# Performance work log

Measured on AMD Instinct MI355X. Metric: run time of the kernel, lower is better.

Reference implementation:

```python
import jax, jax.numpy as jnp
import numpy as np

N_NODES = 100000
N_EDGES = 1600000


def gcn_conv(x, W, b, src, dst, n):
    # PyG GCNConv: x @ W, add self-loops, symmetric deg^{-1/2} normalization,
    # sum-aggregate messages from src into dst, then add bias.
    h = x @ W  # [N, out]
    loops = jnp.arange(n, dtype=src.dtype)
    s = jnp.concatenate([src, loops])
    d = jnp.concatenate([dst, loops])
    deg = jax.ops.segment_sum(jnp.ones_like(d, dtype=h.dtype), d, num_segments=n)
    dinv = 1.0 / jnp.sqrt(deg)  # deg >= 1 thanks to self-loops
    norm = dinv[s] * dinv[d]  # [E + N]
    msg = h[s] * norm[:, None]
    out = jax.ops.segment_sum(msg, d, num_segments=n)
    return out + b


def setup_inputs() -> dict:
    key = jax.random.key(0)
    k1, k2, k3, k4 = jax.random.split(key, 4)
    x = jax.random.normal(k1, (N_NODES, 64), dtype=jnp.float32)
    edge_index = jax.random.randint(k2, (2, N_EDGES), 0, N_NODES, dtype=jnp.int64)
    W1 = jax.random.normal(k3, (64, 32), dtype=jnp.float32) * (1.0 / np.sqrt(64))
    b1 = jnp.zeros((32,), dtype=jnp.float32)
    W2 = jax.random.normal(k4, (32, 16), dtype=jnp.float32) * (1.0 / np.sqrt(32))
    b2 = jnp.zeros((16,), dtype=jnp.float32)
    return {"x": x, "edge_index": edge_index, "W1": W1, "b1": b1, "W2": W2, "b2": b2}


def reference(x, edge_index, W1, b1, W2, b2):
    n = x.shape[0]
    src, dst = edge_index[0], edge_index[1]
    h = gcn_conv(x, W1, b1, src, dst, n)
    h = jax.nn.relu(h)
    h = gcn_conv(h, W2, b2, src, dst, n)
    return jax.nn.log_softmax(h, axis=1)
```

## Files before the change

### kernel.cpp

```cpp
#include <hip/hip_runtime.h>
#include <hip/hip_bf16.h>


#define FEAT_IN 64
#define FEAT_H  32
#define FEAT_O  16
#define MAXNB   512
#define PART_G  256
#define MAXSNB  128

__device__ __forceinline__ float2 upk_bf2(unsigned w) {
    return make_float2(__uint_as_float(w << 16), __uint_as_float(w & 0xFFFF0000u));
}

__global__ void k_hist(const int* __restrict__ dst, int e,
                       int* __restrict__ hist, int G, int NBk) {
    __shared__ int lh[MAXNB];
    int t = threadIdx.x, g = blockIdx.x;
    for (int i = t; i < NBk; i += 256) lh[i] = 0;
    __syncthreads();
    int chunk = (e + G - 1) / G;
    int beg = g * chunk, end = min(e, beg + chunk);
    for (int i = beg + t; i < end; i += 256) atomicAdd(&lh[dst[i] >> 8], 1);
    __syncthreads();
    for (int i = t; i < NBk; i += 256) hist[(size_t)i * G + g] = lh[i];
}

__global__ void k_scan1(const int* __restrict__ in, int* __restrict__ out,
                        int* __restrict__ bsum, int len) {
    __shared__ int s[256];
    int t = threadIdx.x;
    int base = blockIdx.x * 1024 + t * 4;
    int a0 = (base + 0) < len ? in[base + 0] : 0;
    int a1 = (base + 1) < len ? in[base + 1] : 0;
    int a2 = (base + 2) < len ? in[base + 2] : 0;
    int a3 = (base + 3) < len ? in[base + 3] : 0;
    int tsum = a0 + a1 + a2 + a3;
    s[t] = tsum;
    __syncthreads();
    for (int off = 1; off < 256; off <<= 1) {
        int x = (t >= off) ? s[t - off] : 0;
        __syncthreads();
        s[t] += x;
        __syncthreads();
    }
    int ex = s[t] - tsum;
    if (base + 0 < len) out[base + 0] = ex;
    if (base + 1 < len) out[base + 1] = ex + a0;
    if (base + 2 < len) out[base + 2] = ex + a0 + a1;
    if (base + 3 < len) out[base + 3] = ex + a0 + a1 + a2;
    if (t == 255) bsum[blockIdx.x] = s[255];
}

__device__ __forceinline__ void scan_bsum(const int* __restrict__ bsum, int snb,
                                          int* __restrict__ sps, int t) {
    if (t < snb) sps[t] = bsum[t];
    __syncthreads();
    if (t == 0) {
        int acc = 0;
        for (int i = 0; i < snb; ++i) { int v = sps[i]; sps[i] = acc; acc += v; }
    }
    __syncthreads();
}

__global__ void k_partition(const int* __restrict__ src, const int* __restrict__ dst, int e,
                            const int* __restrict__ base, const int* __restrict__ bsum,
                            int snb, int* __restrict__ part, int G, int NBk) {
    __shared__ int cur[MAXNB];
    __shared__ int sps[MAXSNB];
    int t = threadIdx.x, g = blockIdx.x;
    scan_bsum(bsum, snb, sps, t);
    for (int i = t; i < NBk; i += 256) {
        size_t idx = (size_t)i * G + g;
        cur[i] = base[idx] + sps[idx >> 10];
    }
    __syncthreads();
    int chunk = (e + G - 1) / G;
    int beg = g * chunk, end = min(e, beg + chunk);
    for (int i = beg + t; i < end; i += 256) {
        int s_ = src[i], d_ = dst[i];
        int pos = atomicAdd(&cur[d_ >> 8], 1);
        part[pos] = s_ | ((d_ & 255) << 24);
    }
}

__global__ void k_bucket_csr(const int* __restrict__ part, const int* __restrict__ base,
                             const int* __restrict__ bsum, int snb, int e, int G, int NBk,
                             int n, int* __restrict__ row_start, int* __restrict__ col,
                             float* __restrict__ dinv) {
    __shared__ int cnt[256], spre[256], cur[256], ssc[256];
    __shared__ int sps[MAXSNB];
    int t = threadIdx.x, b = blockIdx.x;
    scan_bsum(bsum, snb, sps, t);
    size_t ib = (size_t)b * G;
    size_t ie = (size_t)(b + 1) * G;
    int beg = base[ib] + sps[ib >> 10];
    int end = (b == NBk - 1) ? e : (base[ie] + sps[ie >> 10]);
    cnt[t] = 0; cur[t] = 0;
    __syncthreads();
    for (int j = beg + t; j < end; j += 256) atomicAdd(&cnt[((unsigned)part[j]) >> 24], 1);
    __syncthreads();
    int v = cnt[t];
    ssc[t] = v;
    __syncthreads();
    for (int off = 1; off < 256; off <<= 1) {
        int x = (t >= off) ? ssc[t - off] : 0;
        __syncthreads();
        ssc[t] += x;
        __syncthreads();
    }
    spre[t] = ssc[t] - v;
    int node = b * 256 + t;
    if (node < n) {
        row_start[node] = beg + spre[t];
        dinv[node] = rsqrtf((float)v + 1.0f);
    }
    if (b == NBk - 1 && t == 0) row_start[n] = e;
    __syncthreads();
    for (int j = beg + t; j < end; j += 256) {
        int r = part[j];
        int dl = ((unsigned)r) >> 24;
        int off = atomicAdd(&cur[dl], 1);
        col[beg + spre[dl] + off] = r & 0x00FFFFFF;
    }
}

__global__ void k_gemm1(const float* __restrict__ x, const float* __restrict__ W1,
                        const float* __restrict__ dinv,
                        __hip_bfloat162* __restrict__ h1s2, int n) {
    __shared__ float sW[FEAT_IN * FEAT_H];
    __shared__ float sx[16][FEAT_IN + 1];
    int t = threadIdx.x;
    for (int i = t; i < FEAT_IN * FEAT_H; i += 256) sW[i] = W1[i];
#pragma unroll
    for (int tile = 0; tile < 2; ++tile) {
        int nodeBase = blockIdx.x * 32 + tile * 16;
        __syncthreads();
        {
            int xn = t >> 4, c = t & 15;
            int node = nodeBase + xn;
            if (node < n) {
                float4 v = ((const float4*)x)[(size_t)node * 16 + c];
                sx[xn][c * 4 + 0] = v.x; sx[xn][c * 4 + 1] = v.y;
                sx[xn][c * 4 + 2] = v.z; sx[xn][c * 4 + 3] = v.w;
            }
        }
        __syncthreads();
        int nl = t >> 4, g = t & 15;
        int node = nodeBase + nl;
        if (node < n) {
            float a0 = 0.0f, a1 = 0.0f;
#pragma unroll
            for (int k = 0; k < FEAT_IN; ++k) {
                float s = sx[nl][k];
                a0 += s * sW[k * FEAT_H + 2 * g];
                a1 += s * sW[k * FEAT_H + 2 * g + 1];
            }
            float dv = dinv[node];
            __hip_bfloat162 o;
            o.x = __float2bfloat16(a0 * dv);
            o.y = __float2bfloat16(a1 * dv);
            h1s2[(size_t)node * 16 + g] = o;
        }
    }
}

__global__ void k_gather1_gemm2(const int* __restrict__ row_start, const int* __restrict__ col,
                                const uint4* __restrict__ h1q, const float* __restrict__ W2,
                                const float* __restrict__ b1,
                                const float* __restrict__ dinv,
                                __hip_bfloat162* __restrict__ h2s2, int n) {
    __shared__ float sW[FEAT_H * FEAT_O];
    __shared__ float sb1[FEAT_H];
    __shared__ float sz[64][FEAT_H + 1];
    int t = threadIdx.x;
    for (int i = t; i < FEAT_H * FEAT_O; i += 256) sW[i] = W2[i];
    if (t < FEAT_H) sb1[t] = b1[t];
    __syncthreads();

    int g = t >> 2, l = t & 3;
    int d = blockIdx.x * 64 + g;
    if (d < n) {
        float a[8];
        {
            uint4 u = h1q[(size_t)d * 4 + l];
            float2 p;
            p = upk_bf2(u.x); a[0] = p.x; a[1] = p.y;
            p = upk_bf2(u.y); a[2] = p.x; a[3] = p.y;
            p = upk_bf2(u.z); a[4] = p.x; a[5] = p.y;
            p = upk_bf2(u.w); a[6] = p.x; a[7] = p.y;
        }
        int beg = row_start[d], end = row_start[d + 1];
        int j = beg;
        for (; j + 4 <= end; j += 4) {
            int c0 = col[j + 0], c1 = col[j + 1], c2 = col[j + 2], c3 = col[j + 3];
            uint4 u0 = h1q[(size_t)c0 * 4 + l];
            uint4 u1 = h1q[(size_t)c1 * 4 + l];
            uint4 u2 = h1q[(size_t)c2 * 4 + l];
            uint4 u3 = h1q[(size_t)c3 * 4 + l];
            float2 p;
            p = upk_bf2(u0.x); a[0] += p.x; a[1] += p.y;
            p = upk_bf2(u0.y); a[2] += p.x; a[3] += p.y;
            p = upk_bf2(u0.z); a[4] += p.x; a[5] += p.y;
            p = upk_bf2(u0.w); a[6] += p.x; a[7] += p.y;
            p = upk_bf2(u1.x); a[0] += p.x; a[1] += p.y;
            p = upk_bf2(u1.y); a[2] += p.x; a[3] += p.y;
            p = upk_bf2(u1.z); a[4] += p.x; a[5] += p.y;
            p = upk_bf2(u1.w); a[6] += p.x; a[7] += p.y;
            p = upk_bf2(u2.x); a[0] += p.x; a[1] += p.y;
            p = upk_bf2(u2.y); a[2] += p.x; a[3] += p.y;
            p = upk_bf2(u2.z); a[4] += p.x; a[5] += p.y;
            p = upk_bf2(u2.w); a[6] += p.x; a[7] += p.y;
            p = upk_bf2(u3.x); a[0] += p.x; a[1] += p.y;
            p = upk_bf2(u3.y); a[2] += p.x; a[3] += p.y;
            p = upk_bf2(u3.z); a[4] += p.x; a[5] += p.y;
            p = upk_bf2(u3.w); a[6] += p.x; a[7] += p.y;
        }
        for (; j < end; ++j) {
            uint4 u = h1q[(size_t)col[j] * 4 + l];
            float2 p;
            p = upk_bf2(u.x); a[0] += p.x; a[1] += p.y;
            p = upk_bf2(u.y); a[2] += p.x; a[3] += p.y;
            p = upk_bf2(u.z); a[4] += p.x; a[5] += p.y;
            p = upk_bf2(u.w); a[6] += p.x; a[7] += p.y;
        }
        float dv = dinv[d];
#pragma unroll
        for (int k = 0; k < 8; ++k)
            sz[g][l * 8 + k] = fmaxf(dv * a[k] + sb1[l * 8 + k], 0.0f);
    }
    __syncthreads();
#pragma unroll
    for (int it = 0; it < 2; ++it) {
        int nl = (t >> 3) + it * 32;
        int m = t & 7;
        int node = blockIdx.x * 64 + nl;
        if (node < n) {
            float a0 = 0.0f, a1 = 0.0f;
#pragma unroll
            for (int f = 0; f < FEAT_H; ++f) {
                float z = sz[nl][f];
                a0 += z * sW[f * FEAT_O + 2 * m];
                a1 += z * sW[f * FEAT_O + 2 * m + 1];
            }
            float dv = dinv[node];
            __hip_bfloat162 o;
            o.x = __float2bfloat16(a0 * dv);
            o.y = __float2bfloat16(a1 * dv);
            h2s2[(size_t)node * 8 + m] = o;
        }
    }
}

__global__ void k_gather2_lsm(const int* __restrict__ row_start, const int* __restrict__ col,
                              const uint4* __restrict__ h2q, const float* __restrict__ b2,
                              const float* __restrict__ dinv,
                              float4* __restrict__ out4, int n) {
    __shared__ float sb2[FEAT_O];
    int t = threadIdx.x;
    if (t < FEAT_O) sb2[t] = b2[t];
    __syncthreads();
    int g = t >> 1, h = t & 1;
    int d = blockIdx.x * 128 + g;
    if (d >= n) return;
    float a[8];
    {
        uint4 u = h2q[(size_t)d * 2 + h];
        float2 p;
        p = upk_bf2(u.x); a[0] = p.x; a[1] = p.y;
        p = upk_bf2(u.y); a[2] = p.x; a[3] = p.y;
        p = upk_bf2(u.z); a[4] = p.x; a[5] = p.y;
        p = upk_bf2(u.w); a[6] = p.x; a[7] = p.y;
    }
    int beg = row_start[d], end = row_start[d + 1];
    int j = beg;
    for (; j + 4 <= end; j += 4) {
        int c0 = col[j + 0], c1 = col[j + 1], c2 = col[j + 2], c3 = col[j + 3];
        uint4 u0 = h2q[(size_t)c0 * 2 + h];
        uint4 u1 = h2q[(size_t)c1 * 2 + h];
        uint4 u2 = h2q[(size_t)c2 * 2 + h];
        uint4 u3 = h2q[(size_t)c3 * 2 + h];
        float2 p;
        p = upk_bf2(u0.x); a[0] += p.x; a[1] += p.y;
        p = upk_bf2(u0.y); a[2] += p.x; a[3] += p.y;
        p = upk_bf2(u0.z); a[4] += p.x; a[5] += p.y;
        p = upk_bf2(u0.w); a[6] += p.x; a[7] += p.y;
        p = upk_bf2(u1.x); a[0] += p.x; a[1] += p.y;
        p = upk_bf2(u1.y); a[2] += p.x; a[3] += p.y;
        p = upk_bf2(u1.z); a[4] += p.x; a[5] += p.y;
        p = upk_bf2(u1.w); a[6] += p.x; a[7] += p.y;
        p = upk_bf2(u2.x); a[0] += p.x; a[1] += p.y;
        p = upk_bf2(u2.y); a[2] += p.x; a[3] += p.y;
        p = upk_bf2(u2.z); a[4] += p.x; a[5] += p.y;
        p = upk_bf2(u2.w); a[6] += p.x; a[7] += p.y;
        p = upk_bf2(u3.x); a[0] += p.x; a[1] += p.y;
        p = upk_bf2(u3.y); a[2] += p.x; a[3] += p.y;
        p = upk_bf2(u3.z); a[4] += p.x; a[5] += p.y;
        p = upk_bf2(u3.w); a[6] += p.x; a[7] += p.y;
    }
    for (; j < end; ++j) {
        uint4 u = h2q[(size_t)col[j] * 2 + h];
        float2 p;
        p = upk_bf2(u.x); a[0] += p.x; a[1] += p.y;
        p = upk_bf2(u.y); a[2] += p.x; a[3] += p.y;
        p = upk_bf2(u.z); a[4] += p.x; a[5] += p.y;
        p = upk_bf2(u.w); a[6] += p.x; a[7] += p.y;
    }
    float dv = dinv[d];
    float v[8];
    float mx = -1e30f;
#pragma unroll
    for (int k = 0; k < 8; ++k) {
        v[k] = dv * a[k] + sb2[h * 8 + k];
        mx = fmaxf(mx, v[k]);
    }
    mx = fmaxf(mx, __shfl_xor(mx, 1));
    float ssum = 0.0f;
#pragma unroll
    for (int k = 0; k < 8; ++k) ssum += __expf(v[k] - mx);
    ssum += __shfl_xor(ssum, 1);
    float lg = mx + logf(ssum);
    float4 o0 = { v[0] - lg, v[1] - lg, v[2] - lg, v[3] - lg };
    float4 o1 = { v[4] - lg, v[5] - lg, v[6] - lg, v[7] - lg };
    out4[(size_t)d * 4 + h * 2 + 0] = o0;
    out4[(size_t)d * 4 + h * 2 + 1] = o1;
}

extern "C" void kernel_launch(void* const* d_in, const int* in_sizes, int n_in,
                              void* d_out, int out_size, void* d_ws, size_t ws_size,
                              hipStream_t stream) {
    const float* x  = (const float*)d_in[0];
    const int*   ei = (const int*)d_in[1];
    const float* W1 = (const float*)d_in[2];
    const float* b1 = (const float*)d_in[3];
    const float* W2 = (const float*)d_in[4];
    const float* b2 = (const float*)d_in[5];

    const int n = in_sizes[0] / FEAT_IN;
    const int e = in_sizes[1] / 2;
    const int* src = ei;
    const int* dst = ei + e;
    const int NBk = (n + 255) >> 8;
    const int G = PART_G;
    const int hlen = NBk * G;
    const int snb = (hlen + 1023) / 1024;

    int* part = (int*)d_ws;
    __hip_bfloat162* h1s2 = (__hip_bfloat162*)d_ws;
    int* col  = (int*)d_ws + e;
    __hip_bfloat162* h2s2 = (__hip_bfloat162*)(col + e);
    float* dinv = (float*)(h2s2 + 8 * (size_t)n);
    int* hist      = (int*)(dinv + n);
    int* base      = hist + hlen;
    int* bsum      = base + hlen;
    int* row_start = bsum + MAXSNB;

    k_hist<<<G, 256, 0, stream>>>(dst, e, hist, G, NBk);
    k_scan1<<<snb, 256, 0, stream>>>(hist, base, bsum, hlen);
    k_partition<<<G, 256, 0, stream>>>(src, dst, e, base, bsum, snb, part, G, NBk);
    k_bucket_csr<<<NBk, 256, 0, stream>>>(part, base, bsum, snb, e, G, NBk, n,
                                          row_start, col, dinv);

    k_gemm1<<<(n + 31) / 32, 256, 0, stream>>>(x, W1, dinv, h1s2, n);
    k_gather1_gemm2<<<(n + 63) / 64, 256, 0, stream>>>(row_start, col, (const uint4*)h1s2,
                                                       W2, b1, dinv, h2s2, n);
    k_gather2_lsm<<<(n + 127) / 128, 256, 0, stream>>>(row_start, col, (const uint4*)h2s2,
                                                       b2, dinv, (float4*)d_out, n);
}
```

Before: 184.2 us.

## Replace histogram-scan partition with fixed-capacity buckets and fuse CSR build with GEMM1

The exact prefix-scan partition (hist, scan, partition kernels) is replaced by fixed-capacity buckets of CAP slots each, with offsets claimed by global atomics in a single partition kernel. The CSR-build kernel is fused with the first GEMM, and dinv is recomputed from a per-node (start, count) pair instead of being stored. This cuts the launch count and the global round-trips, but assumes no 256-node bucket receives more than CAP edges. That holds for uniform random graphs but would overflow on skewed degree distributions. The fused kernel also processes 256 nodes of GEMM1 per block on fewer blocks, which may lower parallelism for that stage.

```diff
diff --git a/kernel.cpp b/kernel.cpp
--- a/kernel.cpp
+++ b/kernel.cpp
@@ -7,15 +7,16 @@
 #define FEAT_O  16
 #define MAXNB   512
 #define PART_G  256
-#define MAXSNB  128
+#define CAP     5120
 
 __device__ __forceinline__ float2 upk_bf2(unsigned w) {
     return make_float2(__uint_as_float(w << 16), __uint_as_float(w & 0xFFFF0000u));
 }
 
-__global__ void k_hist(const int* __restrict__ dst, int e,
-                       int* __restrict__ hist, int G, int NBk) {
+__global__ void k_part1(const int* __restrict__ src, const int* __restrict__ dst, int e,
+                        int* __restrict__ gcur, int* __restrict__ part, int G, int NBk) {
     __shared__ int lh[MAXNB];
+    __shared__ int rb[MAXNB];
     int t = threadIdx.x, g = blockIdx.x;
     for (int i = t; i < NBk; i += 256) lh[i] = 0;
     __syncthreads();
@@ -23,80 +24,34 @@
     int beg = g * chunk, end = min(e, beg + chunk);
     for (int i = beg + t; i < end; i += 256) atomicAdd(&lh[dst[i] >> 8], 1);
     __syncthreads();
-    for (int i = t; i < NBk; i += 256) hist[(size_t)i * G + g] = lh[i];
-}
-
-__global__ void k_scan1(const int* __restrict__ in, int* __restrict__ out,
-                        int* __restrict__ bsum, int len) {
-    __shared__ int s[256];
-    int t = threadIdx.x;
-    int base = blockIdx.x * 1024 + t * 4;
-    int a0 = (base + 0) < len ? in[base + 0] : 0;
-    int a1 = (base + 1) < len ? in[base + 1] : 0;
-    int a2 = (base + 2) < len ? in[base + 2] : 0;
-    int a3 = (base + 3) < len ? in[base + 3] : 0;
-    int tsum = a0 + a1 + a2 + a3;
-    s[t] = tsum;
-    __syncthreads();
-    for (int off = 1; off < 256; off <<= 1) {
-        int x = (t >= off) ? s[t - off] : 0;
-        __syncthreads();
-        s[t] += x;
-        __syncthreads();
-    }
-    int ex = s[t] - tsum;
-    if (base + 0 < len) out[base + 0] = ex;
-    if (base + 1 < len) out[base + 1] = ex + a0;
-    if (base + 2 < len) out[base + 2] = ex + a0 + a1;
-    if (base + 3 < len) out[base + 3] = ex + a0 + a1 + a2;
-    if (t == 255) bsum[blockIdx.x] = s[255];
-}
-
-__device__ __forceinline__ void scan_bsum(const int* __restrict__ bsum, int snb,
-                                          int* __restrict__ sps, int t) {
-    if (t < snb) sps[t] = bsum[t];
-    __syncthreads();
-    if (t == 0) {
-        int acc = 0;
-        for (int i = 0; i < snb; ++i) { int v = sps[i]; sps[i] = acc; acc += v; }
-    }
-    __syncthreads();
-}
-
-__global__ void k_partition(const int* __restrict__ src, const int* __restrict__ dst, int e,
-                            const int* __restrict__ base, const int* __restrict__ bsum,
-                            int snb, int* __restrict__ part, int G, int NBk) {
-    __shared__ int cur[MAXNB];
-    __shared__ int sps[MAXSNB];
-    int t = threadIdx.x, g = blockIdx.x;
-    scan_bsum(bsum, snb, sps, t);
     for (int i = t; i < NBk; i += 256) {
-        size_t idx = (size_t)i * G + g;
-        cur[i] = base[idx] + sps[idx >> 10];
-    }
-    __syncthreads();
-    int chunk = (e + G - 1) / G;
-    int beg = g * chunk, end = min(e, beg + chunk);
+        int c = lh[i];
+        rb[i] = c ? atomicAdd(&gcur[i], c) : 0;
+    }
+    __syncthreads();
+    for (int i = t; i < NBk; i += 256) lh[i] = i * CAP + rb[i];
+    __syncthreads();
     for (int i = beg + t; i < end; i += 256) {
         int s_ = src[i], d_ = dst[i];
-        int pos = atomicAdd(&cur[d_ >> 8], 1);
+        int pos = atomicAdd(&lh[d_ >> 8], 1);
         part[pos] = s_ | ((d_ & 255) << 24);
     }
 }
 
-__global__ void k_bucket_csr(const int* __restrict__ part, const int* __restrict__ base,
-                             const int* __restrict__ bsum, int snb, int e, int G, int NBk,
-                             int n, int* __restrict__ row_start, int* __restrict__ col,
-                             float* __restrict__ dinv) {
+__global__ void k_csr_gemm1(const int* __restrict__ part, const int* __restrict__ gcur,
+                            int NBk, int n,
+                            const float* __restrict__ x, const float* __restrict__ W1,
+                            int2* __restrict__ row_info, int* __restrict__ col,
+                            __hip_bfloat162* __restrict__ h1s2) {
     __shared__ int cnt[256], spre[256], cur[256], ssc[256];
-    __shared__ int sps[MAXSNB];
+    __shared__ float sdv[256];
+    __shared__ float sW[FEAT_IN * FEAT_H];
+    __shared__ float sx[16][FEAT_IN + 1];
     int t = threadIdx.x, b = blockIdx.x;
-    scan_bsum(bsum, snb, sps, t);
-    size_t ib = (size_t)b * G;
-    size_t ie = (size_t)(b + 1) * G;
-    int beg = base[ib] + sps[ib >> 10];
-    int end = (b == NBk - 1) ? e : (base[ie] + sps[ie >> 10]);
-    cnt[t] = 0; cur[t] = 0;
+    int beg = b * CAP;
+    int end = beg + gcur[b];
+    cnt[t] = 0;
+    for (int i = t; i < FEAT_IN * FEAT_H; i += 256) sW[i] = W1[i];
     __syncthreads();
     for (int j = beg + t; j < end; j += 256) atomicAdd(&cnt[((unsigned)part[j]) >> 24], 1);
     __syncthreads();
@@ -104,75 +59,64 @@
     ssc[t] = v;
     __syncthreads();
     for (int off = 1; off < 256; off <<= 1) {
-        int x = (t >= off) ? ssc[t - off] : 0;
+        int xv = (t >= off) ? ssc[t - off] : 0;
         __syncthreads();
-        ssc[t] += x;
+        ssc[t] += xv;
         __syncthreads();
     }
     spre[t] = ssc[t] - v;
+    sdv[t] = rsqrtf((float)v + 1.0f);
     int node = b * 256 + t;
-    if (node < n) {
-        row_start[node] = beg + spre[t];
-        dinv[node] = rsqrtf((float)v + 1.0f);
-    }
-    if (b == NBk - 1 && t == 0) row_start[n] = e;
+    if (node < n) row_info[node] = make_int2(beg + spre[t], v);
+    cur[t] = beg + spre[t];
     __syncthreads();
     for (int j = beg + t; j < end; j += 256) {
         int r = part[j];
         int dl = ((unsigned)r) >> 24;
         int off = atomicAdd(&cur[dl], 1);
-        col[beg + spre[dl] + off] = r & 0x00FFFFFF;
-    }
-}
-
-__global__ void k_gemm1(const float* __restrict__ x, const float* __restrict__ W1,
-                        const float* __restrict__ dinv,
-                        __hip_bfloat162* __restrict__ h1s2, int n) {
-    __shared__ float sW[FEAT_IN * FEAT_H];
-    __shared__ float sx[16][FEAT_IN + 1];
-    int t = threadIdx.x;
-    for (int i = t; i < FEAT_IN * FEAT_H; i += 256) sW[i] = W1[i];
-#pragma unroll
-    for (int tile = 0; tile < 2; ++tile) {
-        int nodeBase = blockIdx.x * 32 + tile * 16;
+        col[off] = r & 0x00FFFFFF;
+    }
+#pragma unroll 1
+    for (int tile = 0; tile < 16; ++tile) {
+        int nodeBase = b * 256 + tile * 16;
         __syncthreads();
         {
             int xn = t >> 4, c = t & 15;
-            int node = nodeBase + xn;
-            if (node < n) {
-                float4 v = ((const float4*)x)[(size_t)node * 16 + c];
-                sx[xn][c * 4 + 0] = v.x; sx[xn][c * 4 + 1] = v.y;
-                sx[xn][c * 4 + 2] = v.z; sx[xn][c * 4 + 3] = v.w;
+            int nd = nodeBase + xn;
+            if (nd < n) {
+                float4 vv = ((const float4*)x)[(size_t)nd * 16 + c];
+                sx[xn][c * 4 + 0] = vv.x; sx[xn][c * 4 + 1] = vv.y;
+                sx[xn][c * 4 + 2] = vv.z; sx[xn][c * 4 + 3] = vv.w;
             }
         }
         __syncthreads();
-        int nl = t >> 4, g = t & 15;
-        int node = nodeBase + nl;
-        if (node < n) {
+        int nl = t >> 4, gg = t & 15;
+        int nd = nodeBase + nl;
+        if (nd < n) {
             float a0 = 0.0f, a1 = 0.0f;
 #pragma unroll
             for (int k = 0; k < FEAT_IN; ++k) {
                 float s = sx[nl][k];
-                a0 += s * sW[k * FEAT_H + 2 * g];
-                a1 += s * sW[k * FEAT_H + 2 * g + 1];
+                a0 += s * sW[k * FEAT_H + 2 * gg];
+                a1 += s * sW[k * FEAT_H + 2 * gg + 1];
             }
-            float dv = dinv[node];
+            float dvn = sdv[tile * 16 + nl];
             __hip_bfloat162 o;
-            o.x = __float2bfloat16(a0 * dv);
-            o.y = __float2bfloat16(a1 * dv);
-            h1s2[(size_t)node * 16 + g] = o;
-        }
-    }
-}
-
-__global__ void k_gather1_gemm2(const int* __restrict__ row_start, const int* __restrict__ col,
+            o.x = __float2bfloat16(a0 * dvn);
+            o.y = __float2bfloat16(a1 * dvn);
+            h1s2[(size_t)nd * 16 + gg] = o;
+        }
+    }
+}
+
+__global__ void k_gather1_gemm2(const int2* __restrict__ row_info, const int* __restrict__ col,
                                 const uint4* __restrict__ h1q, const float* __restrict__ W2,
                                 const float* __restrict__ b1,
-                                const float* __restrict__ dinv,
                                 __hip_bfloat162* __restrict__ h2s2, int n) {
     __shared__ float sW[FEAT_H * FEAT_O];
     __shared__ float sb1[FEAT_H];
     __shared__ float sz[64][FEAT_H + 1];
+    __shared__ float sdv[64];
     int t = threadIdx.x;
     for (int i = t; i < FEAT_H * FEAT_O; i += 256) sW[i] = W2[i];
     if (t < FEAT_H) sb1[t] = b1[t];
@@ -190,7 +134,8 @@
             p = upk_bf2(u.z); a[4] = p.x; a[5] = p.y;
             p = upk_bf2(u.w); a[6] = p.x; a[7] = p.y;
         }
-        int beg = row_start[d], end = row_start[d + 1];
+        int2 ri = row_info[d];
+        int beg = ri.x, end = ri.x + ri.y;
         int j = beg;
         for (; j + 4 <= end; j += 4) {
             int c0 = col[j + 0], c1 = col[j + 1], c2 = col[j + 2], c3 = col[j + 3];
@@ -224,7 +169,8 @@
             p = upk_bf2(u.z); a[4] += p.x; a[5] += p.y;
             p = upk_bf2(u.w); a[6] += p.x; a[7] += p.y;
         }
-        float dv = dinv[d];
+        float dv = rsqrtf((float)ri.y + 1.0f);
+        if (l == 0) sdv[g] = dv;
 #pragma unroll
         for (int k = 0; k < 8; ++k)
             sz[g][l * 8 + k] = fmaxf(dv * a[k] + sb1[l * 8 + k], 0.0f);
@@ -243,7 +189,7 @@
                 a0 += z * sW[f * FEAT_O + 2 * m];
                 a1 += z * sW[f * FEAT_O + 2 * m + 1];
             }
-            float dv = dinv[node];
+            float dv = sdv[nl];
             __hip_bfloat162 o;
             o.x = __float2bfloat16(a0 * dv);
             o.y = __float2bfloat16(a1 * dv);
@@ -252,9 +198,8 @@
     }
 }
 
-__global__ void k_gather2_lsm(const int* __restrict__ row_start, const int* __restrict__ col,
+__global__ void k_gather2_lsm(const int2* __restrict__ row_info, const int* __restrict__ col,
                               const uint4* __restrict__ h2q, const float* __restrict__ b2,
-                              const float* __restrict__ dinv,
                               float4* __restrict__ out4, int n) {
     __shared__ float sb2[FEAT_O];
     int t = threadIdx.x;
@@ -272,7 +217,8 @@
         p = upk_bf2(u.z); a[4] = p.x; a[5] = p.y;
         p = upk_bf2(u.w); a[6] = p.x; a[7] = p.y;
     }
-    int beg = row_start[d], end = row_start[d + 1];
+    int2 ri = row_info[d];
+    int beg = ri.x, end = ri.x + ri.y;
     int j = beg;
     for (; j + 4 <= end; j += 4) {
         int c0 = col[j + 0], c1 = col[j + 1], c2 = col[j + 2], c3 = col[j + 3];
@@ -306,7 +252,7 @@
         p = upk_bf2(u.z); a[4] += p.x; a[5] += p.y;
         p = upk_bf2(u.w); a[6] += p.x; a[7] += p.y;
     }
-    float dv = dinv[d];
+    float dv = rsqrtf((float)ri.y + 1.0f);
     float v[8];
     float mx = -1e30f;
 #pragma unroll
@@ -342,28 +288,19 @@
     const int* dst = ei + e;
     const int NBk = (n + 255) >> 8;
     const int G = PART_G;
-    const int hlen = NBk * G;
-    const int snb = (hlen + 1023) / 1024;
-
-    int* part = (int*)d_ws;
-    __hip_bfloat162* h1s2 = (__hip_bfloat162*)d_ws;
-    int* col  = (int*)d_ws + e;
-    __hip_bfloat162* h2s2 = (__hip_bfloat162*)(col + e);
-    float* dinv = (float*)(h2s2 + 8 * (size_t)n);
-    int* hist      = (int*)(dinv + n);
-    int* base      = hist + hlen;
-    int* bsum      = base + hlen;
-    int* row_start = bsum + MAXSNB;
-
-    k_hist<<<G, 256, 0, stream>>>(dst, e, hist, G, NBk);
-    k_scan1<<<snb, 256, 0, stream>>>(hist, base, bsum, hlen);
-    k_partition<<<G, 256, 0, stream>>>(src, dst, e, base, bsum, snb, part, G, NBk);
-    k_bucket_csr<<<NBk, 256, 0, stream>>>(part, base, bsum, snb, e, G, NBk, n,
-                                          row_start, col, dinv);
-
-    k_gemm1<<<(n + 31) / 32, 256, 0, stream>>>(x, W1, dinv, h1s2, n);
-    k_gather1_gemm2<<<(n + 63) / 64, 256, 0, stream>>>(row_start, col, (const uint4*)h1s2,
-                                                       W2, b1, dinv, h2s2, n);
-    k_gather2_lsm<<<(n + 127) / 128, 256, 0, stream>>>(row_start, col, (const uint4*)h2s2,
-                                                       b2, dinv, (float4*)d_out, n);
-}
+
+    int*  gcur = (int*)d_ws;
+    int*  part = gcur + MAXNB;
+    int*  col  = part + (size_t)NBk * CAP;
+    int2* row_info = (int2*)(col + (size_t)NBk * CAP);
+    __hip_bfloat162* h1s2 = (__hip_bfloat162*)(row_info + n);
+    __hip_bfloat162* h2s2 = h1s2 + 16 * (size_t)n;
+
+    hipMemsetAsync(gcur, 0, (size_t)NBk * sizeof(int), stream);
+    k_part1<<<G, 256, 0, stream>>>(src, dst, e, gcur, part, G, NBk);
+    k_csr_gemm1<<<NBk, 256, 0, stream>>>(part, gcur, NBk, n, x, W1, row_info, col, h1s2);
+    k_gather1_gemm2<<<(n + 63) / 64, 256, 0, stream>>>(row_info, col, (const uint4*)h1s2,
+                                                       W2, b1, h2s2, n);
+    k_gather2_lsm<<<(n + 127) / 128, 256, 0, stream>>>(row_info, col, (const uint4*)h2s2,
+                                                       b2, (float4*)d_out, n);
+}
```

Result: slower. 189.0 us (+2.6%).
